# Kernel tuning notes

Measured on AMD Instinct MI355X. Metric: run time of the kernel, lower is better.

The kernel has to match this reference:

```python
import jax, jax.numpy as jnp
import numpy as np

N = 100000   # nodes
E = 800000   # edges (avg degree 8)
IN = 128     # in_dim
H = 128      # hidden_dim
L = 3        # num_layers
EPS = 1e-5   # torch LayerNorm default


def setup_inputs() -> dict:
    key = jax.random.key(0)
    ks = jax.random.split(key, 10)
    s = 0.05
    # DAG edge list: src < dst guarantees acyclicity and node N-1 is a sink.
    rng = np.random.default_rng(0)
    src = rng.integers(0, N - 1, size=E)
    dst = src + 1 + (rng.random(E) * (N - 1 - src)).astype(np.int64)
    return {
        "node_feats": jax.random.normal(ks[0], (N, IN), jnp.float32),
        "src": jnp.asarray(src, jnp.int32),
        "dst": jnp.asarray(dst, jnp.int32),
        "W_in": jax.random.normal(ks[1], (IN, H), jnp.float32) * s,
        "b_in": jnp.zeros((H,), jnp.float32),
        "Ws": jax.random.normal(ks[2], (L, H, H), jnp.float32) * s,
        "bs": jnp.zeros((L, H), jnp.float32),
        "Wn": jax.random.normal(ks[3], (L, H, H), jnp.float32) * s,
        "bn": jnp.zeros((L, H), jnp.float32),
        "Wg": jax.random.normal(ks[4], (L, 2 * H, H), jnp.float32) * s,
        "bg": jnp.zeros((L, H), jnp.float32),
        "gamma": jnp.ones((L, H), jnp.float32),
        "beta": jnp.zeros((L, H), jnp.float32),
        "W_att": jax.random.normal(ks[5], (H, H), jnp.float32) * s,
        "b_att": jnp.zeros((H,), jnp.float32),
        "W_score": jax.random.normal(ks[6], (H, 1), jnp.float32) * s,
        "b_score": jnp.zeros((1,), jnp.float32),
    }


def reference(node_feats, src, dst, W_in, b_in, Ws, bs, Wn, bn, Wg, bg,
              gamma, beta, W_att, b_att, W_score, b_score):
    n = node_feats.shape[0]
    ones_e = jnp.ones(src.shape, node_feats.dtype)
    indeg = jax.ops.segment_sum(ones_e, dst, num_segments=n)          # [N]
    has_pred = (indeg > 0).astype(node_feats.dtype)[:, None]          # [N,1]
    inv_deg = (1.0 / jnp.maximum(indeg, 1.0))[:, None]                # [N,1]
    outdeg = jax.ops.segment_sum(ones_e, src, num_segments=n)
    sink_mask = outdeg == 0                                           # [N]

    h = node_feats @ W_in + b_in                                      # [N,H]
    for i in range(Ws.shape[0]):
        hs = h @ Ws[i] + bs[i]
        # predecessor mean of layer-input h (no within-layer recurrence)
        neigh = jax.ops.segment_sum(h[src], dst, num_segments=n) * inv_deg
        hn = neigh @ Wn[i] + bn[i]
        m = hs + has_pred * hn  # nodes with no preds use m = hs only (bias too)
        gate = jax.nn.sigmoid(jnp.concatenate([h, m], axis=-1) @ Wg[i] + bg[i])
        v = gate * m + (1.0 - gate) * h
        mu = v.mean(-1, keepdims=True)
        var = ((v - mu) ** 2).mean(-1, keepdims=True)
        v = (v - mu) * jax.lax.rsqrt(var + EPS) * gamma[i] + beta[i]
        h = jax.nn.relu(v)

    # attention pooling over sink nodes only
    a = jnp.tanh(h @ W_att + b_att)
    scores = (a @ W_score)[:, 0] + b_score[0]
    scores = jnp.where(sink_mask, scores, -jnp.inf)
    w = jax.nn.softmax(scores, axis=0)  # zero weight on non-sinks
    graph_emb = (w[:, None] * h).sum(0)
    return h, graph_emb
```

## Files before the change

kernel.cpp:

```cpp
#include <hip/hip_runtime.h>
#include <cmath>

typedef unsigned short u16;
typedef unsigned int   u32;
typedef __attribute__((ext_vector_type(8))) short bf16x8;
typedef __attribute__((ext_vector_type(4))) float f32x4;
typedef __attribute__((ext_vector_type(4))) u32   u32x4;

__device__ __forceinline__ float bf2f(u16 u){
    union { u32 i; float f; } x; x.i = ((u32)u) << 16; return x.f;
}
__device__ __forceinline__ u16 f2bf(float f){
    union { float f; u32 i; } x; x.f = f;
    u32 r = x.i + 0x7fffu + ((x.i >> 16) & 1u);
    return (u16)(r >> 16);
}


__global__ void k_count(const int* __restrict__ src, const int* __restrict__ dst,
                        int* cnt, int* notsink, int* pos, int E){
    int e = blockIdx.x*256 + threadIdx.x;
    if (e < E){
        pos[e] = atomicAdd(&cnt[dst[e]], 1);
        notsink[src[e]] = 1;
    }
}

__global__ void k_scan1(const int* __restrict__ in, int* blocksum, int N){
    __shared__ int sh[256];
    int tid = threadIdx.x;
    int base = blockIdx.x*1024 + tid*4;
    int s = 0;
    for (int j=0;j<4;j++){ int i = base+j; s += (i < N) ? in[i] : 0; }
    sh[tid] = s; __syncthreads();
    for (int d=128; d>0; d>>=1){ if (tid < d) sh[tid] += sh[tid+d]; __syncthreads(); }
    if (tid == 0) blocksum[blockIdx.x] = sh[0];
}

__global__ void k_scan2(int* blocksum, int nb){
    if (threadIdx.x == 0){
        int run = 0;
        for (int i=0;i<nb;i++){ int v = blocksum[i]; blocksum[i] = run; run += v; }
    }
}

__global__ void k_scan3(const int* __restrict__ in, const int* __restrict__ blockoff,
                        int* out, float* inv_deg, float* haspred, int N){
    __shared__ int sh[256];
    int tid = threadIdx.x;
    int base = blockIdx.x*1024 + tid*4;
    int e[4]; int s = 0;
    for (int j=0;j<4;j++){ int i = base+j; e[j] = (i < N) ? in[i] : 0; s += e[j]; }
    sh[tid] = s; __syncthreads();
    for (int d=1; d<256; d<<=1){
        int t = (tid >= d) ? sh[tid-d] : 0;
        __syncthreads();
        sh[tid] += t;
        __syncthreads();
    }
    int excl = sh[tid] - s + blockoff[blockIdx.x];
    for (int j=0;j<4;j++){
        int i = base+j;
        if (i < N){
            out[i] = excl; excl += e[j];
            inv_deg[i] = 1.0f / (float)(e[j] > 1 ? e[j] : 1);
            haspred[i] = e[j] > 0 ? 1.0f : 0.0f;
        }
    }
}

__global__ void k_place(const int* __restrict__ src, const int* __restrict__ dst,
                        const int* __restrict__ row_ptr, const int* __restrict__ pos,
                        int* csr_src, int E){
    int e = blockIdx.x*256 + threadIdx.x;
    if (e < E)
        csr_src[row_ptr[dst[e]] + pos[e]] = src[e];
}

__global__ void k_wt_all(const float* __restrict__ W_in, const float* __restrict__ Ws,
                         const float* __restrict__ Wn, const float* __restrict__ Wg,
                         const float* __restrict__ W_att,
                         u16* WT_in, u16* WT_s, u16* WT_n, u16* WT_g, u16* WT_att){
    int i = blockIdx.x*256 + threadIdx.x;
    const float* src; u16* dst; int shift, K, off;
    if (i < 16384)      { src=W_in;  dst=WT_in;  shift=14; K=128; off=i; }
    else if (i < 65536) { src=Ws;    dst=WT_s;   shift=14; K=128; off=i-16384; }
    else if (i < 114688){ src=Wn;    dst=WT_n;   shift=14; K=128; off=i-65536; }
    else if (i < 212992){ src=Wg;    dst=WT_g;   shift=15; K=256; off=i-114688; }
    else if (i < 229376){ src=W_att; dst=WT_att; shift=14; K=128; off=i-212992; }
    else return;
    int mat = off >> shift;
    int w = off & ((1 << shift) - 1);
    int k = w >> 7, n = w & 127;
    dst[(size_t)mat*(K*128) + n*K + k] = f2bf(src[off]);
}


__global__ void k_neigh(const u16* __restrict__ h, const int* __restrict__ row_ptr,
                        const int* __restrict__ indeg, const float* __restrict__ inv_deg,
                        const int* __restrict__ csr_src, u16* __restrict__ neigh, int N){
    int wid  = (blockIdx.x*256 + threadIdx.x) >> 6;
    int lane = threadIdx.x & 63;
    int sub = lane >> 4, sl = lane & 15;
    int node = wid*4 + sub;
    bool valid = node < N;
    int deg   = valid ? indeg[node]   : 0;
    int start = valid ? row_ptr[node] : 0;
    float acc[8] = {0.f,0.f,0.f,0.f,0.f,0.f,0.f,0.f};
    for (int e0 = 0; __any(e0 < deg); e0 += 16){
        int idx = 0;
        if (e0 + sl < deg) idx = csr_src[start + e0 + sl];
        int cnt = deg - e0;
        #pragma unroll
        for (int j = 0; j < 16; j++){
            int sidx = __shfl(idx, (sub << 4) | j);
            if (j < cnt){
                bf16x8 v = *(const bf16x8*)(h + (size_t)sidx*128 + sl*8);
                #pragma unroll
                for (int t=0;t<8;t++) acc[t] += bf2f((u16)v[t]);
            }
        }
    }
    if (valid){
        float iv = inv_deg[node];
        u16 o[8];
        #pragma unroll
        for (int t=0;t<8;t++) o[t] = f2bf(acc[t]*iv);
        *(u32x4*)(neigh + (size_t)node*128 + sl*8) = *(const u32x4*)o;
    }
}


__device__ __forceinline__ void stage_A_bf16(const u16* __restrict__ A, u16 (*lA)[136],
                                             int row0, int n_rows, int tid){
    #pragma unroll
    for (int i=0;i<4;i++){
        int c = i*256 + tid;
        int r = c >> 4, col8 = (c & 15) * 8;
        u32x4 v = {0,0,0,0};
        if (row0 + r < n_rows)
            v = *(const u32x4*)(A + (size_t)(row0 + r)*128 + col8);
        *(u32x4*)&lA[r][col8] = v;
    }
}

__device__ __forceinline__ void stage_A_f32(const float* __restrict__ A, u16 (*lA)[136],
                                            int row0, int n_rows, int tid){
    #pragma unroll
    for (int i=0;i<4;i++){
        int c = i*256 + tid;
        int r = c >> 4, col8 = (c & 15) * 8;
        u16 o[8] = {0,0,0,0,0,0,0,0};
        if (row0 + r < n_rows){
            float4 v0 = *(const float4*)(A + (size_t)(row0 + r)*128 + col8);
            float4 v1 = *(const float4*)(A + (size_t)(row0 + r)*128 + col8 + 4);
            o[0]=f2bf(v0.x); o[1]=f2bf(v0.y); o[2]=f2bf(v0.z); o[3]=f2bf(v0.w);
            o[4]=f2bf(v1.x); o[5]=f2bf(v1.y); o[6]=f2bf(v1.z); o[7]=f2bf(v1.w);
        }
        *(u32x4*)&lA[r][col8] = *(const u32x4*)o;
    }
}

__device__ __forceinline__ void stage_B(const u16* __restrict__ BT, int Ks, int koff0,
                                        u16 (*lB)[136], int tid){
    #pragma unroll
    for (int i=0;i<8;i++){
        int c = i*256 + tid;
        int n = c >> 4, col8 = (c & 15) * 8;
        u32x4 v = *(const u32x4*)(BT + (size_t)n*Ks + koff0 + col8);
        *(u32x4*)&lB[n][col8] = v;
    }
}

__device__ __forceinline__ void stage_B_half(const u16* __restrict__ BT, int Ks, int koff0,
                                             u16 (*lB)[72], int tid){
    #pragma unroll
    for (int i=0;i<4;i++){
        int c = i*256 + tid;
        int n = c >> 3, col8 = (c & 7) * 8;
        *(u32x4*)&lB[n][col8] = *(const u32x4*)(BT + (size_t)n*Ks + koff0 + col8);
    }
}

__device__ __forceinline__ void mfma_tile(const u16 (*lA)[136], const u16 (*lB)[136],
                                          int wave, int lane, f32x4* acc){
    #pragma unroll
    for (int kk=0;kk<4;kk++){
        int koff = kk*32 + (lane >> 4) * 8;
        bf16x8 a = *(const bf16x8*)&lA[wave*16 + (lane & 15)][koff];
        #pragma unroll
        for (int t=0;t<8;t++){
            bf16x8 b = *(const bf16x8*)&lB[t*16 + (lane & 15)][koff];
            acc[t] = __builtin_amdgcn_mfma_f32_16x16x32_bf16(a, b, acc[t], 0, 0, 0);
        }
    }
}

__device__ __forceinline__ void mfma_half(const u16 (*lA)[136], const u16 (*lB)[72],
                                          int wave, int lane, int kbaseA, f32x4* acc){
    #pragma unroll
    for (int kk=0;kk<2;kk++){
        int kw = kk*32 + (lane >> 4) * 8;
        bf16x8 a = *(const bf16x8*)&lA[wave*16 + (lane & 15)][kbaseA + kw];
        #pragma unroll
        for (int t=0;t<8;t++){
            bf16x8 b = *(const bf16x8*)&lB[t*16 + (lane & 15)][kw];
            acc[t] = __builtin_amdgcn_mfma_f32_16x16x32_bf16(a, b, acc[t], 0, 0, 0);
        }
    }
}


__global__ __launch_bounds__(256) void k_gemm_in(
    const float* __restrict__ A, const u16* __restrict__ BT,
    const float* __restrict__ bias, u16* __restrict__ C, int n_rows)
{
    __shared__ u16 lA[64][136];
    __shared__ u16 lB[128][136];
    int tid = threadIdx.x, wave = tid >> 6, lane = tid & 63;
    int row0 = blockIdx.x * 64;
    f32x4 acc[8];
    #pragma unroll
    for (int t=0;t<8;t++) acc[t] = (f32x4){0.f,0.f,0.f,0.f};
    stage_A_f32(A, lA, row0, n_rows, tid);
    stage_B(BT, 128, 0, lB, tid);
    __syncthreads();
    mfma_tile(lA, lB, wave, lane, acc);

    int sl = lane & 15;
    int rbase = wave*16 + (lane >> 4)*4;
    float bc[8];
    #pragma unroll
    for (int t=0;t<8;t++) bc[t] = bias[t*16 + sl];
    for (int r=0;r<4;r++){
        int row = row0 + rbase + r;
        if (row >= n_rows) continue;
        #pragma unroll
        for (int t=0;t<8;t++)
            C[(size_t)row*128 + t*16 + sl] = f2bf(acc[t][r] + bc[t]);
    }
}


__global__ __launch_bounds__(256) void k_layer(
    const u16* __restrict__ H, const u16* __restrict__ Ng,
    const u16* __restrict__ BsT, const u16* __restrict__ BnT,
    const u16* __restrict__ BgT,
    const float* __restrict__ bs, const float* __restrict__ bn,
    const float* __restrict__ bg,
    const float* __restrict__ gamma, const float* __restrict__ beta,
    const float* __restrict__ haspred,
    u16* __restrict__ Hb, float* __restrict__ Hf, int n_rows)
{
    __shared__ u16 lA[64][136];
    __shared__ u16 lM[64][136];
    __shared__ u16 lB[128][72];
    int tid = threadIdx.x, wave = tid >> 6, lane = tid & 63;
    int sl = lane & 15, g16 = lane >> 4;
    int row0 = blockIdx.x * 64;
    f32x4 accs[8], accn[8];
    #pragma unroll
    for (int t=0;t<8;t++){ accs[t] = (f32x4){0.f,0.f,0.f,0.f}; accn[t] = (f32x4){0.f,0.f,0.f,0.f}; }

    stage_A_bf16(H, lA, row0, n_rows, tid);
    stage_B_half(BsT, 128, 0, lB, tid);
    __syncthreads();
    mfma_half(lA, lB, wave, lane, 0, accs);
    __syncthreads();
    stage_B_half(BsT, 128, 64, lB, tid);
    __syncthreads();
    mfma_half(lA, lB, wave, lane, 64, accs);
    __syncthreads();

    stage_A_bf16(Ng, lM, row0, n_rows, tid);
    stage_B_half(BnT, 128, 0, lB, tid);
    __syncthreads();
    mfma_half(lM, lB, wave, lane, 0, accn);
    __syncthreads();
    stage_B_half(BnT, 128, 64, lB, tid);
    __syncthreads();
    mfma_half(lM, lB, wave, lane, 64, accn);
    __syncthreads();

    int rbase = wave*16 + g16*4;
    {
        float bsc[8], bnc[8];
        #pragma unroll
        for (int t=0;t<8;t++){ bsc[t] = bs[t*16 + sl]; bnc[t] = bn[t*16 + sl]; }
        #pragma unroll
        for (int r=0;r<4;r++){
            int row = row0 + rbase + r;
            float hp = (row < n_rows) ? haspred[row] : 0.f;
            #pragma unroll
            for (int t=0;t<8;t++){
                float m = accs[t][r] + bsc[t] + hp*(accn[t][r] + bnc[t]);
                lM[rbase + r][t*16 + sl] = f2bf(m);
            }
        }
    }
    __syncthreads();

    #pragma unroll
    for (int t=0;t<8;t++) accs[t] = (f32x4){0.f,0.f,0.f,0.f};
    stage_B_half(BgT, 256, 0, lB, tid);
    __syncthreads();
    mfma_half(lA, lB, wave, lane, 0, accs);
    __syncthreads();
    stage_B_half(BgT, 256, 64, lB, tid);
    __syncthreads();
    mfma_half(lA, lB, wave, lane, 64, accs);
    __syncthreads();
    stage_B_half(BgT, 256, 128, lB, tid);
    __syncthreads();
    mfma_half(lM, lB, wave, lane, 0, accs);
    __syncthreads();
    stage_B_half(BgT, 256, 192, lB, tid);
    __syncthreads();
    mfma_half(lM, lB, wave, lane, 64, accs);

    float bgc[8], gam[8], bet[8];
    #pragma unroll
    for (int t=0;t<8;t++){
        int col = t*16 + sl;
        bgc[t] = bg[col]; gam[t] = gamma[col]; bet[t] = beta[col];
    }
    for (int r=0;r<4;r++){
        int row = row0 + rbase + r;
        if (row >= n_rows) continue;
        float v[8], s = 0.f;
        #pragma unroll
        for (int t=0;t<8;t++){
            int col = t*16 + sl;
            float x = accs[t][r] + bgc[t];
            float gg = 1.f/(1.f + expf(-x));
            float hv = bf2f(lA[rbase + r][col]);
            float mv = bf2f(lM[rbase + r][col]);
            v[t] = gg*mv + (1.f - gg)*hv;
            s += v[t];
        }
        s += __shfl_xor(s,1); s += __shfl_xor(s,2); s += __shfl_xor(s,4); s += __shfl_xor(s,8);
        float mu = s * (1.f/128.f);
        float q = 0.f;
        #pragma unroll
        for (int t=0;t<8;t++){ float d = v[t]-mu; q += d*d; }
        q += __shfl_xor(q,1); q += __shfl_xor(q,2); q += __shfl_xor(q,4); q += __shfl_xor(q,8);
        float rs = rsqrtf(q*(1.f/128.f) + 1e-5f);
        #pragma unroll
        for (int t=0;t<8;t++){
            size_t idx = (size_t)row*128 + t*16 + sl;
            float o = (v[t]-mu)*rs*gam[t] + bet[t];
            o = o > 0.f ? o : 0.f;
            Hb[idx] = f2bf(o);
            if (Hf) Hf[idx] = o;
        }
    }
}


__global__ __launch_bounds__(256) void k_gemm_att(
    const u16* __restrict__ H, const u16* __restrict__ BT,
    const float* __restrict__ b_att, const float* __restrict__ Wsc,
    const float* __restrict__ bsc, const int* __restrict__ notsink,
    float* __restrict__ scores, int n_rows)
{
    __shared__ u16 lA[64][136];
    __shared__ u16 lB[128][136];
    int tid = threadIdx.x, wave = tid >> 6, lane = tid & 63;
    int row0 = blockIdx.x * 64;
    f32x4 acc[8];
    #pragma unroll
    for (int t=0;t<8;t++) acc[t] = (f32x4){0.f,0.f,0.f,0.f};
    stage_A_bf16(H, lA, row0, n_rows, tid);
    stage_B(BT, 128, 0, lB, tid);
    __syncthreads();
    mfma_tile(lA, lB, wave, lane, acc);

    int sl = lane & 15;
    int rbase = wave*16 + (lane >> 4)*4;
    float bac[8], wc[8];
    #pragma unroll
    for (int t=0;t<8;t++){ bac[t] = b_att[t*16 + sl]; wc[t] = Wsc[t*16 + sl]; }
    float b0 = bsc[0];
    for (int r=0;r<4;r++){
        int row = row0 + rbase + r;
        if (row >= n_rows) continue;
        float p = 0.f;
        #pragma unroll
        for (int t=0;t<8;t++) p += tanhf(acc[t][r] + bac[t]) * wc[t];
        p += __shfl_xor(p,1); p += __shfl_xor(p,2); p += __shfl_xor(p,4); p += __shfl_xor(p,8);
        if (sl == 0)
            scores[row] = (notsink[row] == 0) ? (p + b0) : -INFINITY;
    }
}


__global__ void k_pool1(const u16* __restrict__ h, const float* __restrict__ scores,
                        float* accum, float* part, int N){
    __shared__ float sh[256];
    __shared__ float sw[256];
    int tid = threadIdx.x;
    int col = tid & 127, grp = tid >> 7;
    float acc = 0.f, wsum = 0.f;
    for (int n = blockIdx.x*2 + grp; n < N; n += 512){
        float s = scores[n];
        if (s > -1e30f){
            float w = expf(s);
            acc += w * bf2f(h[(size_t)n*128 + col]);
            if (col == 0) wsum += w;
        }
    }
    sh[tid] = acc; sw[tid] = wsum; __syncthreads();
    if (tid < 128) sw[tid] += sw[tid+128];
    __syncthreads();
    for (int d=64; d>0; d>>=1){ if (tid < d) sw[tid] += sw[tid+d]; __syncthreads(); }
    if (tid < 128) atomicAdd(&accum[col], sh[tid] + sh[tid+128]);
    if (tid == 0) part[blockIdx.x] = sw[0];
}

__global__ void k_pool2(const float* __restrict__ part, const float* __restrict__ accum,
                        float* __restrict__ out){
    __shared__ float sh[256];
    int tid = threadIdx.x;
    sh[tid] = part[tid]; __syncthreads();
    for (int d=128; d>0; d>>=1){ if (tid < d) sh[tid] += sh[tid+d]; __syncthreads(); }
    if (tid < 128) out[tid] = accum[tid] / sh[0];
}


extern "C" void kernel_launch(void* const* d_in, const int* in_sizes, int n_in,
                              void* d_out, int out_size, void* d_ws, size_t ws_size,
                              hipStream_t stream)
{
    const float* node_feats = (const float*)d_in[0];
    const int* src     = (const int*)d_in[1];
    const int* dst     = (const int*)d_in[2];
    const float* W_in    = (const float*)d_in[3];
    const float* b_in    = (const float*)d_in[4];
    const float* Ws      = (const float*)d_in[5];
    const float* bs      = (const float*)d_in[6];
    const float* Wn      = (const float*)d_in[7];
    const float* bn      = (const float*)d_in[8];
    const float* Wg      = (const float*)d_in[9];
    const float* bg      = (const float*)d_in[10];
    const float* gamma   = (const float*)d_in[11];
    const float* beta    = (const float*)d_in[12];
    const float* W_att   = (const float*)d_in[13];
    const float* b_att   = (const float*)d_in[14];
    const float* W_score = (const float*)d_in[15];
    const float* b_score = (const float*)d_in[16];

    const int N = in_sizes[0] / 128;
    const int E = in_sizes[1];

    char* w = (char*)d_ws;
    auto alloc = [&](size_t bytes)->char* {
        char* p = w; w += (bytes + 255) & ~(size_t)255; return p;
    };
    u16* WT_in  = (u16*)alloc(128*128*2);
    u16* WT_s   = (u16*)alloc(3*128*128*2);
    u16* WT_n   = (u16*)alloc(3*128*128*2);
    u16* WT_g   = (u16*)alloc(3*128*256*2);
    u16* WT_att = (u16*)alloc(128*128*2);
    int* cnt      = (int*)alloc((size_t)N*4);
    int* notsink  = (int*)alloc((size_t)N*4);
    float* emb_accum = (float*)alloc(128*4);
    size_t zero_bytes = (size_t)((char*)(emb_accum + 128) - (char*)cnt);
    int* pos      = (int*)alloc((size_t)E*4);
    int* row_ptr  = (int*)alloc((size_t)N*4);
    int* blocksum = (int*)alloc(1024*4);
    int* csr_src  = (int*)alloc((size_t)E*4);
    float* inv_deg = (float*)alloc((size_t)N*4);
    float* haspred = (float*)alloc((size_t)N*4);
    float* scores  = (float*)alloc((size_t)N*4);
    float* part    = (float*)alloc(256*4);
    u16* buf0 = (u16*)alloc((size_t)N*128*2);
    u16* buf1 = (u16*)alloc((size_t)N*128*2);
    u16* bufn = (u16*)alloc((size_t)N*128*2);

    float* h_out   = (float*)d_out;
    float* emb_out = h_out + (size_t)N*128;

    hipMemsetAsync(cnt, 0, zero_bytes, stream);

    k_wt_all<<<(229376+255)/256, 256, 0, stream>>>(W_in, Ws, Wn, Wg, W_att,
                                                   WT_in, WT_s, WT_n, WT_g, WT_att);

    k_count<<<(E+255)/256, 256, 0, stream>>>(src, dst, cnt, notsink, pos, E);

    int nb = (N + 1023) / 1024;
    k_scan1<<<nb, 256, 0, stream>>>(cnt, blocksum, N);
    k_scan2<<<1, 256, 0, stream>>>(blocksum, nb);
    k_scan3<<<nb, 256, 0, stream>>>(cnt, blocksum, row_ptr, inv_deg, haspred, N);
    k_place<<<(E+255)/256, 256, 0, stream>>>(src, dst, row_ptr, pos, csr_src, E);

    int gblk = (N + 63) / 64;
    int nblk = (N + 15) / 16;

    k_gemm_in<<<gblk, 256, 0, stream>>>(node_feats, WT_in, b_in, buf0, N);

    u16* hin = buf0;
    for (int i=0;i<3;i++){
        k_neigh<<<nblk, 256, 0, stream>>>(hin, row_ptr, cnt, inv_deg, csr_src, bufn, N);
        u16* hb  = (hin == buf0) ? buf1 : buf0;
        float* hf = (i == 2) ? h_out : nullptr;
        k_layer<<<gblk, 256, 0, stream>>>(hin, bufn,
                                          WT_s + i*16384, WT_n + i*16384, WT_g + i*32768,
                                          bs + i*128, bn + i*128, bg + i*128,
                                          gamma + i*128, beta + i*128, haspred,
                                          hb, hf, N);
        hin = hb;
    }

    k_gemm_att<<<gblk, 256, 0, stream>>>(hin, WT_att, b_att, W_score, b_score,
                                         notsink, scores, N);
    k_pool1<<<256, 256, 0, stream>>>(hin, scores, emb_accum, part, N);
    k_pool2<<<1, 256, 0, stream>>>(part, emb_accum, emb_out);

    (void)n_in; (void)out_size; (void)ws_size;
}
```

Before: 617.7 us.

## Fold gate projection into precomposed weights and read B operands from global

Precomputes composite weights so the gate pre-activation comes straight from h and the neighbour mean: Ws@Wg_bot is added to the top half of Wg, and Wn@Wg_bot is applied to the neighbour input. The bias contributions are folded into small vectors. Each layer kernel then runs two K=128 products with a 256-wide output and no longer writes m to LDS before a second, dependent gate GEMM. B fragments are now read directly from global/cache instead of being staged through LDS, which removes most barriers but adds many small global loads and more accumulator registers. The composite weights are rounded to bf16 after multiplication, which slightly changes numerics.

```diff
diff --git a/kernel.cpp b/kernel.cpp
--- a/kernel.cpp
+++ b/kernel.cpp
@@ -77,22 +77,59 @@
         csr_src[row_ptr[dst[e]] + pos[e]] = src[e];
 }
 
-__global__ void k_wt_all(const float* __restrict__ W_in, const float* __restrict__ Ws,
-                         const float* __restrict__ Wn, const float* __restrict__ Wg,
-                         const float* __restrict__ W_att,
-                         u16* WT_in, u16* WT_s, u16* WT_n, u16* WT_g, u16* WT_att){
+__global__ void k_wt_plain(const float* __restrict__ W_in, const float* __restrict__ W_att,
+                           const float* __restrict__ Ws, const float* __restrict__ Wn,
+                           u16* WT_in, u16* WT_att, u16* WT1, u16* WT2){
     int i = blockIdx.x*256 + threadIdx.x;
-    const float* src; u16* dst; int shift, K, off;
-    if (i < 16384)      { src=W_in;  dst=WT_in;  shift=14; K=128; off=i; }
-    else if (i < 65536) { src=Ws;    dst=WT_s;   shift=14; K=128; off=i-16384; }
-    else if (i < 114688){ src=Wn;    dst=WT_n;   shift=14; K=128; off=i-65536; }
-    else if (i < 212992){ src=Wg;    dst=WT_g;   shift=15; K=256; off=i-114688; }
-    else if (i < 229376){ src=W_att; dst=WT_att; shift=14; K=128; off=i-212992; }
-    else return;
-    int mat = off >> shift;
-    int w = off & ((1 << shift) - 1);
-    int k = w >> 7, n = w & 127;
-    dst[(size_t)mat*(K*128) + n*K + k] = f2bf(src[off]);
+    if (i < 32768){
+        const float* srcm = (i < 16384) ? W_in : W_att;
+        u16* dstm = (i < 16384) ? WT_in : WT_att;
+        int w = i & 16383, n = w >> 7, k = w & 127;
+        dstm[n*128 + k] = f2bf(srcm[k*128 + n]);
+    } else {
+        int off = i - 32768;
+        int m  = off / 49152;
+        int w  = off % 49152;
+        int l  = w >> 14, ww = w & 16383;
+        int n  = ww >> 7, k = ww & 127;
+        const float* srcm = m ? Wn : Ws;
+        u16* dstm = m ? WT2 : WT1;
+        dstm[(size_t)l*32768 + n*128 + k] = f2bf(srcm[(size_t)l*16384 + k*128 + n]);
+    }
+}
+
+__global__ void k_wt_comp(const float* __restrict__ Ws, const float* __restrict__ Wn,
+                          const float* __restrict__ Wg,
+                          const float* __restrict__ bs, const float* __restrict__ bn,
+                          u16* WT1, u16* WT2, float* vb){
+    __shared__ float cols[2][128];
+    int l = blockIdx.x / 129;
+    int b = blockIdx.x % 129;
+    const float* Wgb = Wg + (size_t)l*32768 + 16384;
+    int tid = threadIdx.x;
+    if (b == 128){
+        int n = tid & 127;
+        const float* bv = (tid < 128) ? (bs + l*128) : (bn + l*128);
+        float acc = 0.f;
+        for (int j=0;j<128;j++) acc += bv[j] * Wgb[j*128 + n];
+        vb[l*256 + (tid>>7)*128 + n] = acc;
+        return;
+    }
+    int m  = b >> 6;
+    int n0 = (b & 63) * 2;
+    int nn = tid >> 7, k = tid & 127;
+    cols[tid>>7][tid&127] = Wgb[(size_t)(tid&127)*128 + n0 + (tid>>7)];
+    __syncthreads();
+    const float* A = (m ? Wn : Ws) + (size_t)l*16384;
+    float acc = 0.f;
+    for (int j=0;j<128;j++) acc += A[k*128 + j] * cols[nn][j];
+    int n = n0 + nn;
+    if (m == 0){
+        acc += Wg[(size_t)l*32768 + k*128 + n];
+        WT1[(size_t)l*32768 + (size_t)(128+n)*128 + k] = f2bf(acc);
+    } else {
+        WT2[(size_t)l*32768 + (size_t)(128+n)*128 + k] = f2bf(acc);
+    }
 }
 
 
@@ -172,16 +209,6 @@
     }
 }
 
-__device__ __forceinline__ void stage_B_half(const u16* __restrict__ BT, int Ks, int koff0,
-                                             u16 (*lB)[72], int tid){
-    #pragma unroll
-    for (int i=0;i<4;i++){
-        int c = i*256 + tid;
-        int n = c >> 3, col8 = (c & 7) * 8;
-        *(u32x4*)&lB[n][col8] = *(const u32x4*)(BT + (size_t)n*Ks + koff0 + col8);
-    }
-}
-
 __device__ __forceinline__ void mfma_tile(const u16 (*lA)[136], const u16 (*lB)[136],
                                           int wave, int lane, f32x4* acc){
     #pragma unroll
@@ -191,20 +218,6 @@
         #pragma unroll
         for (int t=0;t<8;t++){
             bf16x8 b = *(const bf16x8*)&lB[t*16 + (lane & 15)][koff];
-            acc[t] = __builtin_amdgcn_mfma_f32_16x16x32_bf16(a, b, acc[t], 0, 0, 0);
-        }
-    }
-}
-
-__device__ __forceinline__ void mfma_half(const u16 (*lA)[136], const u16 (*lB)[72],
-                                          int wave, int lane, int kbaseA, f32x4* acc){
-    #pragma unroll
-    for (int kk=0;kk<2;kk++){
-        int kw = kk*32 + (lane >> 4) * 8;
-        bf16x8 a = *(const bf16x8*)&lA[wave*16 + (lane & 15)][kbaseA + kw];
-        #pragma unroll
-        for (int t=0;t<8;t++){
-            bf16x8 b = *(const bf16x8*)&lB[t*16 + (lane & 15)][kw];
             acc[t] = __builtin_amdgcn_mfma_f32_16x16x32_bf16(a, b, acc[t], 0, 0, 0);
         }
     }
@@ -244,98 +257,69 @@
 
 __global__ __launch_bounds__(256) void k_layer(
     const u16* __restrict__ H, const u16* __restrict__ Ng,
-    const u16* __restrict__ BsT, const u16* __restrict__ BnT,
-    const u16* __restrict__ BgT,
+    const u16* __restrict__ WT1, const u16* __restrict__ WT2,
     const float* __restrict__ bs, const float* __restrict__ bn,
     const float* __restrict__ bg,
+    const float* __restrict__ vb1, const float* __restrict__ vb2,
     const float* __restrict__ gamma, const float* __restrict__ beta,
     const float* __restrict__ haspred,
     u16* __restrict__ Hb, float* __restrict__ Hf, int n_rows)
 {
     __shared__ u16 lA[64][136];
-    __shared__ u16 lM[64][136];
-    __shared__ u16 lB[128][72];
+    __shared__ u16 lN[64][136];
     int tid = threadIdx.x, wave = tid >> 6, lane = tid & 63;
     int sl = lane & 15, g16 = lane >> 4;
     int row0 = blockIdx.x * 64;
-    f32x4 accs[8], accn[8];
-    #pragma unroll
-    for (int t=0;t<8;t++){ accs[t] = (f32x4){0.f,0.f,0.f,0.f}; accn[t] = (f32x4){0.f,0.f,0.f,0.f}; }
-
-    stage_A_bf16(H, lA, row0, n_rows, tid);
-    stage_B_half(BsT, 128, 0, lB, tid);
+
+    f32x4 acc[16];
+    #pragma unroll
+    for (int t=0;t<16;t++) acc[t] = (f32x4){0.f,0.f,0.f,0.f};
+
+    stage_A_bf16(H,  lA, row0, n_rows, tid);
+    stage_A_bf16(Ng, lN, row0, n_rows, tid);
     __syncthreads();
-    mfma_half(lA, lB, wave, lane, 0, accs);
-    __syncthreads();
-    stage_B_half(BsT, 128, 64, lB, tid);
-    __syncthreads();
-    mfma_half(lA, lB, wave, lane, 64, accs);
-    __syncthreads();
-
-    stage_A_bf16(Ng, lM, row0, n_rows, tid);
-    stage_B_half(BnT, 128, 0, lB, tid);
-    __syncthreads();
-    mfma_half(lM, lB, wave, lane, 0, accn);
-    __syncthreads();
-    stage_B_half(BnT, 128, 64, lB, tid);
-    __syncthreads();
-    mfma_half(lM, lB, wave, lane, 64, accn);
-    __syncthreads();
+
+    const u16* B1 = WT1 + (size_t)sl*128;
+    const u16* B2 = WT2 + (size_t)sl*128;
+    #pragma unroll
+    for (int kk=0;kk<4;kk++){
+        int koff = kk*32 + g16*8;
+        bf16x8 a1 = *(const bf16x8*)&lA[wave*16 + sl][koff];
+        bf16x8 a2 = *(const bf16x8*)&lN[wave*16 + sl][koff];
+        #pragma unroll
+        for (int t=0;t<16;t++){
+            bf16x8 b = *(const bf16x8*)(B1 + (size_t)t*2048 + koff);
+            acc[t] = __builtin_amdgcn_mfma_f32_16x16x32_bf16(a1, b, acc[t], 0, 0, 0);
+        }
+        #pragma unroll
+        for (int t=0;t<16;t++){
+            bf16x8 b = *(const bf16x8*)(B2 + (size_t)t*2048 + koff);
+            acc[t] = __builtin_amdgcn_mfma_f32_16x16x32_bf16(a2, b, acc[t], 0, 0, 0);
+        }
+    }
 
     int rbase = wave*16 + g16*4;
-    {
-        float bsc[8], bnc[8];
-        #pragma unroll
-        for (int t=0;t<8;t++){ bsc[t] = bs[t*16 + sl]; bnc[t] = bn[t*16 + sl]; }
-        #pragma unroll
-        for (int r=0;r<4;r++){
-            int row = row0 + rbase + r;
-            float hp = (row < n_rows) ? haspred[row] : 0.f;
-            #pragma unroll
-            for (int t=0;t<8;t++){
-                float m = accs[t][r] + bsc[t] + hp*(accn[t][r] + bnc[t]);
-                lM[rbase + r][t*16 + sl] = f2bf(m);
-            }
-        }
-    }
-    __syncthreads();
-
-    #pragma unroll
-    for (int t=0;t<8;t++) accs[t] = (f32x4){0.f,0.f,0.f,0.f};
-    stage_B_half(BgT, 256, 0, lB, tid);
-    __syncthreads();
-    mfma_half(lA, lB, wave, lane, 0, accs);
-    __syncthreads();
-    stage_B_half(BgT, 256, 64, lB, tid);
-    __syncthreads();
-    mfma_half(lA, lB, wave, lane, 64, accs);
-    __syncthreads();
-    stage_B_half(BgT, 256, 128, lB, tid);
-    __syncthreads();
-    mfma_half(lM, lB, wave, lane, 0, accs);
-    __syncthreads();
-    stage_B_half(BgT, 256, 192, lB, tid);
-    __syncthreads();
-    mfma_half(lM, lB, wave, lane, 64, accs);
-
-    float bgc[8], gam[8], bet[8];
+    float bM[8], bnl[8], bG[8], vb2l[8], gam[8], bet[8];
     #pragma unroll
     for (int t=0;t<8;t++){
-        int col = t*16 + sl;
-        bgc[t] = bg[col]; gam[t] = gamma[col]; bet[t] = beta[col];
+        int c = t*16 + sl;
+        bM[t] = bs[c]; bnl[t] = bn[c];
+        bG[t] = bg[c] + vb1[c]; vb2l[t] = vb2[c];
+        gam[t] = gamma[c]; bet[t] = beta[c];
     }
     for (int r=0;r<4;r++){
         int row = row0 + rbase + r;
         if (row >= n_rows) continue;
+        float hp = haspred[row];
         float v[8], s = 0.f;
         #pragma unroll
         for (int t=0;t<8;t++){
-            int col = t*16 + sl;
-            float x = accs[t][r] + bgc[t];
+            int c = t*16 + sl;
+            float m = acc[t][r]   + bM[t] + hp*bnl[t];
+            float x = acc[t+8][r] + bG[t] + hp*vb2l[t];
             float gg = 1.f/(1.f + expf(-x));
-            float hv = bf2f(lA[rbase + r][col]);
-            float mv = bf2f(lM[rbase + r][col]);
-            v[t] = gg*mv + (1.f - gg)*hv;
+            float hv = bf2f(lA[rbase + r][c]);
+            v[t] = gg*m + (1.f - gg)*hv;
             s += v[t];
         }
         s += __shfl_xor(s,1); s += __shfl_xor(s,2); s += __shfl_xor(s,4); s += __shfl_xor(s,8);
@@ -457,10 +441,10 @@
         char* p = w; w += (bytes + 255) & ~(size_t)255; return p;
     };
     u16* WT_in  = (u16*)alloc(128*128*2);
-    u16* WT_s   = (u16*)alloc(3*128*128*2);
-    u16* WT_n   = (u16*)alloc(3*128*128*2);
-    u16* WT_g   = (u16*)alloc(3*128*256*2);
     u16* WT_att = (u16*)alloc(128*128*2);
+    u16* WT1    = (u16*)alloc(3*256*128*2);
+    u16* WT2    = (u16*)alloc(3*256*128*2);
+    float* vb   = (float*)alloc(3*256*4);
     int* cnt      = (int*)alloc((size_t)N*4);
     int* notsink  = (int*)alloc((size_t)N*4);
     float* emb_accum = (float*)alloc(128*4);
@@ -482,8 +466,8 @@
 
     hipMemsetAsync(cnt, 0, zero_bytes, stream);
 
-    k_wt_all<<<(229376+255)/256, 256, 0, stream>>>(W_in, Ws, Wn, Wg, W_att,
-                                                   WT_in, WT_s, WT_n, WT_g, WT_att);
+    k_wt_plain<<<512, 256, 0, stream>>>(W_in, W_att, Ws, Wn, WT_in, WT_att, WT1, WT2);
+    k_wt_comp<<<3*129, 256, 0, stream>>>(Ws, Wn, Wg, bs, bn, WT1, WT2, vb);
 
     k_count<<<(E+255)/256, 256, 0, stream>>>(src, dst, cnt, notsink, pos, E);
 
@@ -504,8 +488,9 @@
         u16* hb  = (hin == buf0) ? buf1 : buf0;
         float* hf = (i == 2) ? h_out : nullptr;
         k_layer<<<gblk, 256, 0, stream>>>(hin, bufn,
-                                          WT_s + i*16384, WT_n + i*16384, WT_g + i*32768,
+                                          WT1 + i*32768, WT2 + i*32768,
                                           bs + i*128, bn + i*128, bg + i*128,
+                                          vb + i*256, vb + i*256 + 128,
                                           gamma + i*128, beta + i*128, haspred,
                                           hb, hf, N);
         hin = hb;
```

Result: slower. 923.8 us (+49.6%).
